# Kernel optimization log

Measured on AMD Instinct MI355X. Metric: run time of the kernel, lower is better.

## Reference

```python
import jax, jax.numpy as jnp
import numpy as np

ENCODER_DIM = 2048
DECODER_DIM = 512
ATTENTION_DIM = 512
BATCH = 512
NUM_PIXELS = 196


def setup_inputs() -> dict:
    key = jax.random.key(0)
    k = jax.random.split(key, 8)
    s_e = 1.0 / np.sqrt(ENCODER_DIM)
    s_d = 1.0 / np.sqrt(DECODER_DIM)
    s_a = 1.0 / np.sqrt(ATTENTION_DIM)
    return {
        "encoder_out": jax.random.normal(k[0], (BATCH, NUM_PIXELS, ENCODER_DIM), jnp.float32),
        "decoder_hidden": jax.random.normal(k[1], (BATCH, DECODER_DIM), jnp.float32),
        "W_enc": jax.random.uniform(k[2], (ENCODER_DIM, ATTENTION_DIM), jnp.float32, -s_e, s_e),
        "b_enc": jax.random.uniform(k[3], (ATTENTION_DIM,), jnp.float32, -s_e, s_e),
        "W_dec": jax.random.uniform(k[4], (DECODER_DIM, ATTENTION_DIM), jnp.float32, -s_d, s_d),
        "b_dec": jax.random.uniform(k[5], (ATTENTION_DIM,), jnp.float32, -s_d, s_d),
        "W_full": jax.random.uniform(k[6], (ATTENTION_DIM,), jnp.float32, -s_a, s_a),
        "b_full": jax.random.uniform(k[7], (), jnp.float32, -s_a, s_a),
    }


def reference(encoder_out, decoder_hidden, W_enc, b_enc, W_dec, b_dec, W_full, b_full):
    # att1: [B, P, A], att2: [B, A]
    att1 = jnp.einsum('bpe,ea->bpa', encoder_out, W_enc) + b_enc
    att2 = decoder_hidden @ W_dec + b_dec
    # scores: [B, P]
    scores = jnp.einsum('bpa,a->bp', jnp.tanh(att1 + att2[:, None, :]), W_full) + b_full
    alpha = jax.nn.softmax(scores, axis=1)
    context = jnp.einsum('bpe,bp->be', encoder_out, alpha)
    return context, alpha
```

## Files before the change

### kernel.cpp

```cpp
#include <hip/hip_runtime.h>
#include <hip/hip_bf16.h>
#include <stdint.h>

#define BATCH 512
#define PIX   196
#define EDIM  2048
#define DDIM  512
#define ADIM  512
#define MROWS (BATCH*PIX)

#define BM 128
#define BN 128
#define BK 32
#define NKT (EDIM/BK)

typedef __attribute__((ext_vector_type(8))) short bf16x8;
typedef __attribute__((ext_vector_type(4))) float f32x4;

#define GLL16(g, lptr) __builtin_amdgcn_global_load_lds( \
    (const __attribute__((address_space(1))) void*)(g),  \
    (__attribute__((address_space(3))) void*)(lptr), 16, 0, 0)

static __device__ __forceinline__ unsigned short f2bf(float f) {
  union { float f; uint32_t u; } v; v.f = f;
  uint32_t u = v.u;
  return (unsigned short)((u + 0x7FFFu + ((u >> 16) & 1u)) >> 16);
}

static __device__ __forceinline__ bf16x8 pack8(float4 a, float4 b) {
  bf16x8 r;
  r[0] = (short)f2bf(a.x); r[1] = (short)f2bf(a.y);
  r[2] = (short)f2bf(a.z); r[3] = (short)f2bf(a.w);
  r[4] = (short)f2bf(b.x); r[5] = (short)f2bf(b.y);
  r[6] = (short)f2bf(b.z); r[7] = (short)f2bf(b.w);
  return r;
}

__global__ void k_transpose_wenc(const float* __restrict__ W,
                                 unsigned short* __restrict__ Bt) {
  __shared__ float tile[32][33];
  const int kt = blockIdx.x;
  const int nt = blockIdx.y;
  const int tx = threadIdx.x, ty = threadIdx.y;
#pragma unroll
  for (int j = 0; j < 4; j++)
    tile[ty + 8*j][tx] = W[(size_t)(kt*32 + ty + 8*j)*ADIM + nt*32 + tx];
  __syncthreads();
#pragma unroll
  for (int j = 0; j < 4; j++)
    Bt[(size_t)(nt*32 + ty + 8*j)*EDIM + kt*32 + tx] = f2bf(tile[tx][ty + 8*j]);
}

__global__ void k_att2(const float* __restrict__ H, const float* __restrict__ Wd,
                       const float* __restrict__ bd, float* __restrict__ att2) {
  __shared__ float h[DDIM];
  const int b = blockIdx.x;
  const int t = threadIdx.x;
  h[t]       = H[(size_t)b*DDIM + t];
  h[t + 256] = H[(size_t)b*DDIM + t + 256];
  __syncthreads();
  float a0 = 0.f, a1 = 0.f;
#pragma unroll 8
  for (int k = 0; k < DDIM; k++) {
    const float hv = h[k];
    a0 += hv * Wd[(size_t)k*ADIM + t];
    a1 += hv * Wd[(size_t)k*ADIM + t + 256];
  }
  att2[(size_t)b*ADIM + t]       = a0 + bd[t];
  att2[(size_t)b*ADIM + t + 256] = a1 + bd[t + 256];
}

__global__ __launch_bounds__(256, 3) void k_gemm_scores(
    const float* __restrict__ enc,
    const unsigned short* __restrict__ Bt,
    const float* __restrict__ b_enc,
    const float* __restrict__ att2,
    const float* __restrict__ W_full,
    float* __restrict__ scores)
{
  __shared__ float Asf[2][BM][BK];
  __shared__ unsigned short Bsb[2][BN][BK];
  __shared__ float sc[BM];

  const int t   = threadIdx.x;
  const int l   = t & 63;
  const int wid = t >> 6;
  const int wr  = wid >> 1, wc = wid & 1;

  const int orig = blockIdx.x;
  const int tile = (orig & 7) * 392 + (orig >> 3);
  const int bm0 = (tile >> 2) * BM;
  const int bn0 = (tile & 3) * BN;

  if (t < BM) sc[t] = 0.f;

#define STAGE(bufi, kt) do {                                                  \
    _Pragma("unroll")                                                         \
    for (int j = 0; j < 4; j++) {                                             \
      const int c   = j*256 + t;                                              \
      const int row = c >> 3;                                                 \
      const int cir = (c & 7) ^ (row & 7);                                    \
      GLL16(enc + (size_t)(bm0 + row)*EDIM + (kt)*BK + cir*4,                 \
            (char*)(&Asf[bufi][0][0]) + (j*4 + wid)*1024);                    \
    }                                                                         \
    _Pragma("unroll")                                                         \
    for (int j = 0; j < 2; j++) {                                             \
      const int c   = j*256 + t;                                              \
      const int row = c >> 2;                                                 \
      GLL16(Bt + (size_t)(bn0 + row)*EDIM + (kt)*BK + (c & 3)*8,              \
            (char*)(&Bsb[bufi][0][0]) + (j*4 + wid)*1024);                    \
    }                                                                         \
  } while (0)

  f32x4 acc[4][4] = {};

  STAGE(0, 0);
  __syncthreads();

  int cur = 0;
  for (int kt = 0; kt < NKT; kt++) {
    if (kt + 1 < NKT) STAGE(cur ^ 1, kt + 1);

    bf16x8 af[4], bfr[4];
#pragma unroll
    for (int mi = 0; mi < 4; mi++) {
      const int r = wr*64 + mi*16 + (l & 15);
      const int g = (l >> 4) * 2;
      const float4 fa = *(const float4*)((const char*)&Asf[cur][0][0]
                            + r*128 + ((g    ) ^ (r & 7))*16);
      const float4 fb = *(const float4*)((const char*)&Asf[cur][0][0]
                            + r*128 + ((g + 1) ^ (r & 7))*16);
      af[mi] = pack8(fa, fb);
    }
#pragma unroll
    for (int ni = 0; ni < 4; ni++)
      bfr[ni] = *(const bf16x8*)(&Bsb[cur][wc*64 + ni*16 + (l & 15)][(l >> 4) * 8]);

#pragma unroll
    for (int mi = 0; mi < 4; mi++)
#pragma unroll
      for (int ni = 0; ni < 4; ni++)
        acc[mi][ni] = __builtin_amdgcn_mfma_f32_16x16x32_bf16(af[mi], bfr[ni], acc[mi][ni], 0, 0, 0);

    __syncthreads();
    cur ^= 1;
  }

  const int lr = l >> 4;
  const int lc = l & 15;
  float be[4], wf[4];
  int colv[4];
#pragma unroll
  for (int ni = 0; ni < 4; ni++) {
    colv[ni] = bn0 + wc*64 + ni*16 + lc;
    be[ni] = b_enc[colv[ni]];
    wf[ni] = W_full[colv[ni]];
  }
#pragma unroll
  for (int mi = 0; mi < 4; mi++) {
#pragma unroll
    for (int e = 0; e < 4; e++) {
      const int row_l = wr*64 + mi*16 + lr*4 + e;
      const unsigned gr = (unsigned)(bm0 + row_l);
      const unsigned b  = gr / 196u;
      float s = 0.f;
#pragma unroll
      for (int ni = 0; ni < 4; ni++) {
        const float v = acc[mi][ni][e] + be[ni] + att2[(size_t)b*ADIM + colv[ni]];
        s += tanhf(v) * wf[ni];
      }
      s += __shfl_xor(s, 1); s += __shfl_xor(s, 2);
      s += __shfl_xor(s, 4); s += __shfl_xor(s, 8);
      if (lc == 0) atomicAdd(&sc[row_l], s);
    }
  }
  __syncthreads();
  if (t < BM) atomicAdd(&scores[bm0 + t], sc[t]);
}

__global__ void k_softmax(float* __restrict__ sa) {
  __shared__ float red[256];
  const int b = blockIdx.x, t = threadIdx.x;
  const float v = (t < PIX) ? sa[(size_t)b*PIX + t] : -1e30f;
  red[t] = v; __syncthreads();
  for (int s2 = 128; s2 > 0; s2 >>= 1) {
    if (t < s2) red[t] = fmaxf(red[t], red[t + s2]);
    __syncthreads();
  }
  const float m = red[0]; __syncthreads();
  const float e = (t < PIX) ? __expf(v - m) : 0.f;
  red[t] = e; __syncthreads();
  for (int s2 = 128; s2 > 0; s2 >>= 1) {
    if (t < s2) red[t] += red[t + s2];
    __syncthreads();
  }
  const float inv = 1.f / red[0];
  if (t < PIX) sa[(size_t)b*PIX + t] = e * inv;
}

__global__ __launch_bounds__(512) void k_context(
    const float* __restrict__ enc, const float* __restrict__ alpha,
    float* __restrict__ ctx) {
  __shared__ float al[PIX];
  const int b = blockIdx.x, t = threadIdx.x;
  if (t < PIX) al[t] = alpha[(size_t)b*PIX + t];
  __syncthreads();
  const float4* e4 = (const float4*)(enc + (size_t)b * PIX * EDIM);
  float4 acc = {0.f, 0.f, 0.f, 0.f};
#pragma unroll 4
  for (int p = 0; p < PIX; p++) {
    const float4 v = e4[(size_t)p * (EDIM/4) + t];
    const float a = al[p];
    acc.x += v.x * a; acc.y += v.y * a; acc.z += v.z * a; acc.w += v.w * a;
  }
  ((float4*)(ctx + (size_t)b * EDIM))[t] = acc;
}

extern "C" void kernel_launch(void* const* d_in, const int* in_sizes, int n_in,
                              void* d_out, int out_size, void* d_ws, size_t ws_size,
                              hipStream_t stream) {
  (void)in_sizes; (void)n_in; (void)out_size; (void)ws_size;
  const float* enc   = (const float*)d_in[0];
  const float* hid   = (const float*)d_in[1];
  const float* Wenc  = (const float*)d_in[2];
  const float* benc  = (const float*)d_in[3];
  const float* Wdec  = (const float*)d_in[4];
  const float* bdec  = (const float*)d_in[5];
  const float* Wfull = (const float*)d_in[6];

  unsigned short* Bt = (unsigned short*)d_ws;
  float* att2 = (float*)((char*)d_ws + (size_t)ADIM * EDIM * 2);
  float* ctx   = (float*)d_out;
  float* alpha = (float*)d_out + (size_t)BATCH * EDIM;

  hipMemsetAsync(alpha, 0, (size_t)MROWS * sizeof(float), stream);
  k_transpose_wenc<<<dim3(64, 16), dim3(32, 8), 0, stream>>>(Wenc, Bt);
  k_att2<<<BATCH, 256, 0, stream>>>(hid, Wdec, bdec, att2);
  k_gemm_scores<<<3136, 256, 0, stream>>>(enc, Bt, benc, att2, Wfull, alpha);
  k_softmax<<<BATCH, 256, 0, stream>>>(alpha);
  k_context<<<BATCH, 512, 0, stream>>>(enc, alpha, ctx);
}
```

Before: 667.5 us.

## Triple-buffer GEMM LDS staging with explicit vmcnt waits and vector bf16 convert

Moves the fused score GEMM from double-buffered to triple-buffered LDS staging, issuing loads three K-tiles ahead. Each iteration waits with counted s_waitcnt vmcnt on only the oldest stage instead of a full __syncthreads. The manual fp32-to-bf16 rounding is replaced by a vector convertvector, which may lower to hardware conversion instructions. The larger LDS footprint lowers the launch_bounds occupancy hint from 3 to 2 blocks per CU, trading occupancy for deeper prefetch.

Result: slower. 769.3 us (+15.3%).

```diff
diff --git a/kernel.cpp b/kernel.cpp
--- a/kernel.cpp
+++ b/kernel.cpp
@@ -15,6 +15,8 @@
 #define NKT (EDIM/BK)
 
 typedef __attribute__((ext_vector_type(8))) short bf16x8;
+typedef __attribute__((ext_vector_type(8))) float f32x8;
+typedef __attribute__((ext_vector_type(8))) __bf16 bf16v8;
 typedef __attribute__((ext_vector_type(4))) float f32x4;
 
 #define GLL16(g, lptr) __builtin_amdgcn_global_load_lds( \
@@ -27,12 +29,11 @@
   return (unsigned short)((u + 0x7FFFu + ((u >> 16) & 1u)) >> 16);
 }
 
-static __device__ __forceinline__ bf16x8 pack8(float4 a, float4 b) {
+static __device__ __forceinline__ bf16x8 cvt8(float4 a, float4 b) {
+  f32x8 v = {a.x, a.y, a.z, a.w, b.x, b.y, b.z, b.w};
+  bf16v8 c = __builtin_convertvector(v, bf16v8);
   bf16x8 r;
-  r[0] = (short)f2bf(a.x); r[1] = (short)f2bf(a.y);
-  r[2] = (short)f2bf(a.z); r[3] = (short)f2bf(a.w);
-  r[4] = (short)f2bf(b.x); r[5] = (short)f2bf(b.y);
-  r[6] = (short)f2bf(b.z); r[7] = (short)f2bf(b.w);
+  __builtin_memcpy(&r, &c, 16);
   return r;
 }
 
@@ -70,7 +71,7 @@
   att2[(size_t)b*ADIM + t + 256] = a1 + bd[t + 256];
 }
 
-__global__ __launch_bounds__(256, 3) void k_gemm_scores(
+__global__ __launch_bounds__(256, 2) void k_gemm_scores(
     const float* __restrict__ enc,
     const unsigned short* __restrict__ Bt,
     const float* __restrict__ b_enc,
@@ -78,8 +79,8 @@
     const float* __restrict__ W_full,
     float* __restrict__ scores)
 {
-  __shared__ float Asf[2][BM][BK];
-  __shared__ unsigned short Bsb[2][BN][BK];
+  __shared__ float Asf[3][BM][BK];
+  __shared__ unsigned short Bsb[3][BN][BK];
   __shared__ float sc[BM];
 
   const int t   = threadIdx.x;
@@ -115,26 +116,31 @@
   f32x4 acc[4][4] = {};
 
   STAGE(0, 0);
-  __syncthreads();
-
-  int cur = 0;
+  STAGE(1, 1);
+  STAGE(2, 2);
+
   for (int kt = 0; kt < NKT; kt++) {
-    if (kt + 1 < NKT) STAGE(cur ^ 1, kt + 1);
+    const int buf = kt - (kt / 3) * 3;
+
+    if (kt < NKT - 2)      asm volatile("s_waitcnt vmcnt(12)" ::: "memory");
+    else if (kt == NKT - 2) asm volatile("s_waitcnt vmcnt(6)" ::: "memory");
+    else                    asm volatile("s_waitcnt vmcnt(0)" ::: "memory");
+    __builtin_amdgcn_s_barrier();
 
     bf16x8 af[4], bfr[4];
 #pragma unroll
     for (int mi = 0; mi < 4; mi++) {
       const int r = wr*64 + mi*16 + (l & 15);
       const int g = (l >> 4) * 2;
-      const float4 fa = *(const float4*)((const char*)&Asf[cur][0][0]
+      const float4 fa = *(const float4*)((const char*)&Asf[buf][0][0]
                             + r*128 + ((g    ) ^ (r & 7))*16);
-      const float4 fb = *(const float4*)((const char*)&Asf[cur][0][0]
+      const float4 fb = *(const float4*)((const char*)&Asf[buf][0][0]
                             + r*128 + ((g + 1) ^ (r & 7))*16);
-      af[mi] = pack8(fa, fb);
+      af[mi] = cvt8(fa, fb);
     }
 #pragma unroll
     for (int ni = 0; ni < 4; ni++)
-      bfr[ni] = *(const bf16x8*)(&Bsb[cur][wc*64 + ni*16 + (l & 15)][(l >> 4) * 8]);
+      bfr[ni] = *(const bf16x8*)(&Bsb[buf][wc*64 + ni*16 + (l & 15)][(l >> 4) * 8]);
 
 #pragma unroll
     for (int mi = 0; mi < 4; mi++)
@@ -142,8 +148,10 @@
       for (int ni = 0; ni < 4; ni++)
         acc[mi][ni] = __builtin_amdgcn_mfma_f32_16x16x32_bf16(af[mi], bfr[ni], acc[mi][ni], 0, 0, 0);
 
-    __syncthreads();
-    cur ^= 1;
+    asm volatile("s_waitcnt lgkmcnt(0)" ::: "memory");
+    __builtin_amdgcn_s_barrier();
+
+    if (kt + 3 < NKT) STAGE(buf, kt + 3);
   }
 
   const int lr = l >> 4;
```
